# Kernel optimization log

Measured on AMD Instinct MI355X. Metric: run time of the kernel, lower is better.

## Reference

```python
import jax, jax.numpy as jnp
import numpy as np

DIM, NH = 256, 8
B, L_INNER, L_LEAF, L_ROOT = 16, 128, 64, 16


def mha(q, k, v, wi, bi, wo, bo, nh=NH):
    # Faithful torch.nn.MultiheadAttention (batch_first): packed in_proj, q scaled by head_dim**-0.5.
    E = q.shape[-1]
    hd = E // nh
    wq, wk, wv = wi[:E], wi[E:2 * E], wi[2 * E:]
    bq, bk, bv = bi[:E], bi[E:2 * E], bi[2 * E:]

    def proj(x, w, b):
        Bx, Lx, _ = x.shape
        return (x @ w.T + b).reshape(Bx, Lx, nh, hd).transpose(0, 2, 1, 3)  # [B,H,L,hd]

    qh = proj(q, wq, bq) * (float(hd) ** -0.5)
    kh = proj(k, wk, bk)
    vh = proj(v, wv, bv)
    attn = jax.nn.softmax(jnp.einsum('bhqd,bhkd->bhqk', qh, kh), axis=-1)
    o = jnp.einsum('bhqk,bhkd->bhqd', attn, vh).transpose(0, 2, 1, 3).reshape(q.shape)
    return o @ wo.T + bo


def setup_inputs() -> dict:
    key = jax.random.key(0)
    ks = jax.random.split(key, 10)
    return {
        'leaf': jax.random.normal(ks[0], (B * L_INNER, L_LEAF, DIM), jnp.float32),
        'inner': jax.random.normal(ks[1], (B, L_INNER, DIM), jnp.float32),
        'root': jax.random.normal(ks[2], (B, L_ROOT, DIM), jnp.float32),
        'w_in': jax.random.normal(ks[3], (7, 3 * DIM, DIM), jnp.float32) * 0.02,
        'b_in': jax.random.normal(ks[4], (7, 3 * DIM), jnp.float32) * 0.02,
        'w_out': jax.random.normal(ks[5], (7, DIM, DIM), jnp.float32) * 0.02,
        'b_out': jax.random.normal(ks[6], (7, DIM), jnp.float32) * 0.02,
        'weight_leaf': jax.random.normal(ks[7], (2,), jnp.float32),
        'weight_inner': jax.random.normal(ks[8], (3,), jnp.float32),
        'weight_root': jax.random.normal(ks[9], (2,), jnp.float32),
    }


def reference(leaf, inner, root, w_in, b_in, w_out, b_out, weight_leaf, weight_inner, weight_root):
    # param slots: 0 leaf_parents, 1 leaf_siblings, 2 inner_parents, 3 inner_siblings,
    #              4 inner_children, 5 root_siblings, 6 root_children (constructed but UNUSED, as in source)
    inner_flat = inner.reshape(-1, 1, DIM)  # [B*L_inner, 1, dim]

    leaf_p = mha(leaf, inner_flat, inner_flat, w_in[0], b_in[0], w_out[0], b_out[0])
    leaf_s = mha(leaf, leaf, leaf, w_in[1], b_in[1], w_out[1], b_out[1])
    wl = jax.nn.softmax(weight_leaf)
    leaf_out = wl[0] * leaf_p + wl[1] * leaf_s

    inner_p = mha(inner, root, root, w_in[2], b_in[2], w_out[2], b_out[2])
    inner_s = mha(inner, inner, inner, w_in[3], b_in[3], w_out[3], b_out[3])
    inner_c = mha(inner_flat, leaf, leaf, w_in[4], b_in[4], w_out[4], b_out[4]).reshape(inner.shape)
    wi_ = jax.nn.softmax(weight_inner)
    inner_out = wi_[0] * inner_p + wi_[1] * inner_s + wi_[2] * inner_c

    root_s = mha(root, root, root, w_in[5], b_in[5], w_out[5], b_out[5])
    # source bug reproduced: root_c also uses attn_root_siblings (slot 5)
    root_c = mha(root, inner, inner, w_in[5], b_in[5], w_out[5], b_out[5])
    wr = jax.nn.softmax(weight_root)
    root_out = wr[0] * root_s + wr[1] * root_c

    return (leaf_out, inner_out, root_out)
```

## Files before the change

kernel.cpp:

```cpp
#include <hip/hip_runtime.h>
#include <hip/hip_bf16.h>
#include <cstdint>


#define DIM 256
#define NH 8
#define HD 32

static constexpr float SCALE = 0.17677669529663687f;

typedef __bf16 bf16x8 __attribute__((ext_vector_type(8)));
typedef __bf16 bf16x4 __attribute__((ext_vector_type(4)));
typedef float  f32x4  __attribute__((ext_vector_type(4)));

__device__ __forceinline__ float dot4(const float4 a, const float4 b) {
    return a.x * b.x + a.y * b.y + a.z * b.z + a.w * b.w;
}

__global__ __launch_bounds__(256) void cvt_f2b(const float* __restrict__ s,
                                               __bf16* __restrict__ d, int n) {
    int i = (blockIdx.x * 256 + threadIdx.x) * 4;
    if (i < n) {
        float4 v = *(const float4*)(s + i);
        d[i + 0] = (__bf16)v.x; d[i + 1] = (__bf16)v.y;
        d[i + 2] = (__bf16)v.z; d[i + 3] = (__bf16)v.w;
    }
}

__device__ void mega2_body(int g,
    const float* __restrict__ X, const float* __restrict__ inner,
    const __bf16* __restrict__ W1b, const float* __restrict__ Bi1,
    const __bf16* __restrict__ W4kvb, const float* __restrict__ W4q,
    const float* __restrict__ Bi4, __bf16* __restrict__ O1,
    float* __restrict__ Oc, char* __restrict__ smem)
{
    const int xcd  = g & 7;
    const int idx  = g >> 3;
    const int b    = xcd * 256 + (idx >> 2);
    const int hg   = idx & 3;
    const int tid  = threadIdx.x;
    const int wid  = tid >> 6;
    const int lane = tid & 63;
    const int lr   = lane & 15;
    const int lk   = (lane >> 4) * 8;
    const int prow = (lane >> 4) * 4;

    __bf16* Xs  = (__bf16*)smem;
    __bf16* Pw  = (__bf16*)(smem + wid * 2304);
    float* qpart = (float*)(smem + 9216);
    float* qv    = qpart + 256;
    float* psm   = qv + 64;
    float* opart = psm + 128;
    __bf16* Qs  = (__bf16*)(smem + 33792);
    __bf16* Ks  = (__bf16*)(smem + 43008);
    __bf16* Vt  = (__bf16*)(smem + 52224);
    __bf16* K4t = (__bf16*)(smem + 61440);
    __bf16* V4t = (__bf16*)(smem + 70656);

    {
        const float* xb = X + (size_t)b * 64 * DIM;
#pragma unroll
        for (int it = 0; it < 16; ++it) {
            const int e4 = it * 1024 + tid * 4;
            const f32x4 v = __builtin_nontemporal_load((const f32x4*)(xb + e4));
            bf16x4 t4;
            t4[0] = (__bf16)v[0]; t4[1] = (__bf16)v[1];
            t4[2] = (__bf16)v[2]; t4[3] = (__bf16)v[3];
            const int row = e4 >> 8, col = e4 & 255;
            *(bf16x4*)(Xs + row * 264 + col) = t4;
        }
    }
    __syncthreads();

    bf16x8 af[4][8];
#pragma unroll
    for (int tg = 0; tg < 4; ++tg)
#pragma unroll
        for (int kk = 0; kk < 8; ++kk)
            af[tg][kk] = *(const bf16x8*)(Xs + (size_t)(tg * 16 + lr) * 264 + kk * 32 + lk);

    {
        auto wsrc = [&](int t) -> const __bf16* {
            if (t < 12) {
                const int sec = t >> 2, sub = t & 3;
                return W1b + (size_t)(sec * 256 + hg * 64 + sub * 16) * DIM;
            }
            const int u = t - 12, sec = u >> 2, sub = u & 3;
            return W4kvb + (size_t)(sec * 256 + hg * 64 + sub * 16) * DIM;
        };
        const size_t boff = (size_t)lr * DIM + lk;
        const int t0w = wid * 5;
        bf16x8 bw[8], bn[8];
        {
            const __bf16* p = wsrc(t0w) + boff;
#pragma unroll
            for (int kk = 0; kk < 8; ++kk) bw[kk] = *(const bf16x8*)(p + kk * 32);
        }
        for (int i = 0; i < 5; ++i) {
            const int t = t0w + i;
            if (i + 1 < 5) {
                const __bf16* p = wsrc(t + 1) + boff;
#pragma unroll
                for (int kk = 0; kk < 8; ++kk) bn[kk] = *(const bf16x8*)(p + kk * 32);
            }
            f32x4 acc0 = {0.f,0.f,0.f,0.f}, acc1 = {0.f,0.f,0.f,0.f};
            f32x4 acc2 = {0.f,0.f,0.f,0.f}, acc3 = {0.f,0.f,0.f,0.f};
#pragma unroll
            for (int kk = 0; kk < 8; ++kk) {
                acc0 = __builtin_amdgcn_mfma_f32_16x16x32_bf16(af[0][kk], bw[kk], acc0, 0, 0, 0);
                acc1 = __builtin_amdgcn_mfma_f32_16x16x32_bf16(af[1][kk], bw[kk], acc1, 0, 0, 0);
                acc2 = __builtin_amdgcn_mfma_f32_16x16x32_bf16(af[2][kk], bw[kk], acc2, 0, 0, 0);
                acc3 = __builtin_amdgcn_mfma_f32_16x16x32_bf16(af[3][kk], bw[kk], acc3, 0, 0, 0);
            }
            f32x4 accT[4] = { acc0, acc1, acc2, acc3 };
            const int sub = t & 3;
            const int col = sub * 16 + lr;
            if (t < 4) {
                const float bias = Bi1[hg * 64 + sub * 16 + lr];
#pragma unroll
                for (int tg = 0; tg < 4; ++tg)
#pragma unroll
                    for (int r = 0; r < 4; ++r)
                        Qs[(size_t)(tg * 16 + prow + r) * 72 + col] =
                            (__bf16)((accT[tg][r] + bias) * SCALE);
            } else if (t < 8) {
                const float bias = Bi1[256 + hg * 64 + sub * 16 + lr];
#pragma unroll
                for (int tg = 0; tg < 4; ++tg)
#pragma unroll
                    for (int r = 0; r < 4; ++r)
                        Ks[(size_t)(tg * 16 + prow + r) * 72 + col] =
                            (__bf16)(accT[tg][r] + bias);
            } else if (t < 12) {
                const float bias = Bi1[512 + hg * 64 + sub * 16 + lr];
#pragma unroll
                for (int tg = 0; tg < 4; ++tg) {
                    bf16x4 pv;
#pragma unroll
                    for (int r = 0; r < 4; ++r) pv[r] = (__bf16)(accT[tg][r] + bias);
                    *(bf16x4*)(Vt + (size_t)col * 72 + tg * 16 + prow) = pv;
                }
            } else if (t < 16) {
                const float bias = Bi4[256 + hg * 64 + sub * 16 + lr];
#pragma unroll
                for (int tg = 0; tg < 4; ++tg) {
                    bf16x4 pv;
#pragma unroll
                    for (int r = 0; r < 4; ++r) pv[r] = (__bf16)(accT[tg][r] + bias);
                    *(bf16x4*)(K4t + (size_t)col * 72 + tg * 16 + prow) = pv;
                }
            } else {
                const float bias = Bi4[512 + hg * 64 + sub * 16 + lr];
#pragma unroll
                for (int tg = 0; tg < 4; ++tg) {
                    bf16x4 pv;
#pragma unroll
                    for (int r = 0; r < 4; ++r) pv[r] = (__bf16)(accT[tg][r] + bias);
                    *(bf16x4*)(V4t + (size_t)col * 72 + tg * 16 + prow) = pv;
                }
            }
#pragma unroll
            for (int kk = 0; kk < 8; ++kk) bw[kk] = bn[kk];
        }
    }
    __syncthreads();

    {
        const int o = tid & 63, part = tid >> 6;
        const float4* wr = (const float4*)(W4q + (size_t)(hg * 64 + o) * DIM + part * 64);
        const float4* xr = (const float4*)(inner + (size_t)b * DIM + part * 64);
        float accq = 0.f;
#pragma unroll
        for (int k = 0; k < 16; ++k) accq += dot4(xr[k], wr[k]);
        qpart[part * 64 + o] = accq;
    }
    __syncthreads();

    if (tid < 64)
        qv[tid] = (qpart[tid] + qpart[64 + tid] + qpart[128 + tid] + qpart[192 + tid]
                   + Bi4[hg * 64 + tid]) * SCALE;

    const int hh = wid >> 1;
    const int qh = wid & 1;
    f32x4 s[2][4];
    {
        bf16x8 kb[4];
#pragma unroll
        for (int kt = 0; kt < 4; ++kt)
            kb[kt] = *(const bf16x8*)(Ks + (size_t)(kt * 16 + lr) * 72 + hh * 32 + lk);
#pragma unroll
        for (int q2 = 0; q2 < 2; ++q2) {
            const int qt = qh * 2 + q2;
            const bf16x8 qa = *(const bf16x8*)(Qs + (size_t)(qt * 16 + lr) * 72 + hh * 32 + lk);
#pragma unroll
            for (int kt = 0; kt < 4; ++kt) {
                f32x4 z = {0.f, 0.f, 0.f, 0.f};
                s[q2][kt] = __builtin_amdgcn_mfma_f32_16x16x32_bf16(qa, kb[kt], z, 0, 0, 0);
            }
        }
    }
#pragma unroll
    for (int q2 = 0; q2 < 2; ++q2) {
#pragma unroll
        for (int r = 0; r < 4; ++r) {
            float m = fmaxf(fmaxf(s[q2][0][r], s[q2][1][r]), fmaxf(s[q2][2][r], s[q2][3][r]));
#pragma unroll
            for (int off = 1; off < 16; off <<= 1) m = fmaxf(m, __shfl_xor(m, off));
            const float p0 = __expf(s[q2][0][r] - m), p1 = __expf(s[q2][1][r] - m);
            const float p2 = __expf(s[q2][2][r] - m), p3 = __expf(s[q2][3][r] - m);
            float t = p0 + p1 + p2 + p3;
#pragma unroll
            for (int off = 1; off < 16; off <<= 1) t += __shfl_xor(t, off);
            const float inv = 1.0f / t;
            s[q2][0][r] = p0 * inv; s[q2][1][r] = p1 * inv;
            s[q2][2][r] = p2 * inv; s[q2][3][r] = p3 * inv;
        }
    }
    {
        bf16x8 vb[2][2];
#pragma unroll
        for (int dt = 0; dt < 2; ++dt)
#pragma unroll
            for (int ks = 0; ks < 2; ++ks)
                vb[dt][ks] = *(const bf16x8*)(Vt + (size_t)(hh * 32 + dt * 16 + lr) * 72 + ks * 32 + lk);
#pragma unroll
        for (int q2 = 0; q2 < 2; ++q2) {
            const int qt = qh * 2 + q2;
#pragma unroll
            for (int kt = 0; kt < 4; ++kt)
#pragma unroll
                for (int r = 0; r < 4; ++r)
                    Pw[(size_t)(prow + r) * 72 + kt * 16 + lr] = (__bf16)s[q2][kt][r];
            bf16x8 pa[2];
#pragma unroll
            for (int ks = 0; ks < 2; ++ks)
                pa[ks] = *(const bf16x8*)(Pw + (size_t)lr * 72 + ks * 32 + lk);
#pragma unroll
            for (int dt = 0; dt < 2; ++dt) {
                f32x4 o = {0.f, 0.f, 0.f, 0.f};
#pragma unroll
                for (int ks = 0; ks < 2; ++ks)
                    o = __builtin_amdgcn_mfma_f32_16x16x32_bf16(pa[ks], vb[dt][ks], o, 0, 0, 0);
                const int colO = (hg * 2 + hh) * 32 + dt * 16 + lr;
#pragma unroll
                for (int r = 0; r < 4; ++r)
                    __builtin_nontemporal_store((__bf16)o[r],
                        &O1[((size_t)b * 64 + qt * 16 + prow + r) * DIM + colO]);
            }
        }
    }
    __syncthreads();

    if (wid < 2) {
        const int j = lane;
        float sv = 0.f;
#pragma unroll
        for (int d = 0; d < 32; ++d)
            sv += qv[wid * 32 + d] * (float)K4t[(size_t)(wid * 32 + d) * 72 + j];
        float m = sv;
#pragma unroll
        for (int off = 1; off < 64; off <<= 1) m = fmaxf(m, __shfl_xor(m, off));
        const float p = __expf(sv - m);
        float t = p;
#pragma unroll
        for (int off = 1; off < 64; off <<= 1) t += __shfl_xor(t, off);
        psm[wid * 64 + j] = p / t;
    }
    __syncthreads();

    if (tid < 128) {
        const int o = tid & 63, hf = tid >> 6;
        const int ho = o >> 5;
        float acc2 = 0.f;
#pragma unroll
        for (int j = 0; j < 32; ++j)
            acc2 += psm[ho * 64 + hf * 32 + j] * (float)V4t[(size_t)o * 72 + hf * 32 + j];
        opart[hf * 64 + o] = acc2;
    }
    __syncthreads();
    if (tid < 64)
        Oc[(size_t)b * DIM + hg * 64 + tid] = opart[tid] + opart[64 + tid];
}

__device__ void leafp_mfma_body(int bid, const float* __restrict__ inner,
    const __bf16* __restrict__ Wv0b, const __bf16* __restrict__ Wo0b,
    const float* __restrict__ b_in0, const float* __restrict__ b_out0,
    float* __restrict__ tP, char* __restrict__ smem)
{
    __bf16* tV = (__bf16*)smem;
    __bf16* Bs = (__bf16*)(smem + 33792);
    const int tid  = threadIdx.x;
    const int wid  = tid >> 6;
    const int lane = tid & 63;
    const int lr   = lane & 15;
    const int lk   = (lane >> 4) * 8;
    const int prow = (lane >> 4) * 4;
    const int tok0 = wid * 16 + prow;
    const int srow = tid >> 5;
    const int scol = (tid & 31) * 8;

    bf16x8 a[8];
    {
        const float* xrow = inner + ((size_t)bid * 64 + wid * 16 + lr) * DIM + lk;
#pragma unroll
        for (int k = 0; k < 8; ++k) {
            float4 v0 = *(const float4*)(xrow + k * 32);
            float4 v1 = *(const float4*)(xrow + k * 32 + 4);
            bf16x8 t;
            t[0] = (__bf16)v0.x; t[1] = (__bf16)v0.y; t[2] = (__bf16)v0.z; t[3] = (__bf16)v0.w;
            t[4] = (__bf16)v1.x; t[5] = (__bf16)v1.y; t[6] = (__bf16)v1.z; t[7] = (__bf16)v1.w;
            a[k] = t;
        }
    }

    {
        bf16x8 g0 = *(const bf16x8*)(Wv0b + (size_t)srow * DIM + scol);
        bf16x8 g1 = *(const bf16x8*)(Wv0b + (size_t)(8 + srow) * DIM + scol);
        *(bf16x8*)(Bs + srow * 264 + scol) = g0;
        *(bf16x8*)(Bs + (8 + srow) * 264 + scol) = g1;
    }
    __syncthreads();
    for (int t = 0; t < 16; ++t) {
        const int cur = t & 1;
        const __bf16* Bc = Bs + cur * 4224;
        bf16x8 g0, g1;
        if (t + 1 < 16) {
            const __bf16* p = Wv0b + (size_t)((t + 1) * 16) * DIM;
            g0 = *(const bf16x8*)(p + (size_t)srow * DIM + scol);
            g1 = *(const bf16x8*)(p + (size_t)(8 + srow) * DIM + scol);
        }
        f32x4 acc = {0.f, 0.f, 0.f, 0.f};
#pragma unroll
        for (int k = 0; k < 8; ++k)
            acc = __builtin_amdgcn_mfma_f32_16x16x32_bf16(
                a[k], *(const bf16x8*)(Bc + lr * 264 + k * 32 + lk), acc, 0, 0, 0);
        const float bias = b_in0[512 + t * 16 + lr];
#pragma unroll
        for (int r = 0; r < 4; ++r)
            tV[(size_t)(tok0 + r) * 264 + t * 16 + lr] = (__bf16)(acc[r] + bias);
        if (t + 1 < 16) {
            __bf16* Bn = Bs + (cur ^ 1) * 4224;
            *(bf16x8*)(Bn + srow * 264 + scol) = g0;
            *(bf16x8*)(Bn + (8 + srow) * 264 + scol) = g1;
        }
        __syncthreads();
    }

    bf16x8 a2[8];
#pragma unroll
    for (int k = 0; k < 8; ++k)
        a2[k] = *(const bf16x8*)(tV + (size_t)(wid * 16 + lr) * 264 + k * 32 + lk);
    {
        bf16x8 g0 = *(const bf16x8*)(Wo0b + (size_t)srow * DIM + scol);
        bf16x8 g1 = *(const bf16x8*)(Wo0b + (size_t)(8 + srow) * DIM + scol);
        *(bf16x8*)(Bs + srow * 264 + scol) = g0;
        *(bf16x8*)(Bs + (8 + srow) * 264 + scol) = g1;
    }
    __syncthreads();
    for (int t = 0; t < 16; ++t) {
        const int cur = t & 1;
        const __bf16* Bc = Bs + cur * 4224;
        bf16x8 g0, g1;
        if (t + 1 < 16) {
            const __bf16* p = Wo0b + (size_t)((t + 1) * 16) * DIM;
            g0 = *(const bf16x8*)(p + (size_t)srow * DIM + scol);
            g1 = *(const bf16x8*)(p + (size_t)(8 + srow) * DIM + scol);
        }
        f32x4 acc = {0.f, 0.f, 0.f, 0.f};
#pragma unroll
        for (int k = 0; k < 8; ++k)
            acc = __builtin_amdgcn_mfma_f32_16x16x32_bf16(
                a2[k], *(const bf16x8*)(Bc + lr * 264 + k * 32 + lk), acc, 0, 0, 0);
        const float bo = b_out0[t * 16 + lr];
#pragma unroll
        for (int r = 0; r < 4; ++r)
            tP[((size_t)bid * 64 + wid * 16 + prow + r) * DIM + t * 16 + lr] = acc[r] + bo;
        if (t + 1 < 16) {
            __bf16* Bn = Bs + (cur ^ 1) * 4224;
            *(bf16x8*)(Bn + srow * 264 + scol) = g0;
            *(bf16x8*)(Bn + (8 + srow) * 264 + scol) = g1;
        }
        __syncthreads();
    }
}

template <int LQ, int LK, int RQ>
__device__ void attn_body(int bx, const float* __restrict__ Xq,
                          const float* __restrict__ Xkv,
                          const float* __restrict__ Wi, const float* __restrict__ Bi,
                          float* __restrict__ O, float* __restrict__ sm)
{
    const int b   = bx >> 3;
    const int h   = bx & 7;
    const int tid = threadIdx.x;

    float* KsP = sm;
    float* VsP = KsP + LK * 33;
    float* QsP = VsP + LK * 33;
    float* SP  = QsP + LQ * 33;

    const float* xq  = Xq  + (size_t)b * LQ * DIM;
    const float* xkv = Xkv + (size_t)b * LK * DIM;

    {
        const int col   = tid & 63;
        const int which = col >> 5;
        const int d     = col & 31;
        const int row   = DIM + which * DIM + h * HD + d;
        const float4* wr = (const float4*)(Wi + (size_t)row * DIM);
        const float bias = Bi[row];
        constexpr int TT = LK / 4;
        float acc[TT];
#pragma unroll
        for (int i = 0; i < TT; ++i) acc[i] = 0.f;
        const int t0 = tid >> 6;
        for (int k4 = 0; k4 < DIM / 4; ++k4) {
            const float4 w = wr[k4];
#pragma unroll
            for (int i = 0; i < TT; ++i) {
                const int t = t0 + 4 * i;
                const float4 aa = ((const float4*)(xkv + (size_t)t * DIM))[k4];
                acc[i] += dot4(aa, w);
            }
        }
#pragma unroll
        for (int i = 0; i < TT; ++i) {
            const int t = t0 + 4 * i;
            if (which == 0) KsP[t * 33 + d] = acc[i] + bias;
            else            VsP[t * 33 + d] = acc[i] + bias;
        }
    }
    {
        constexpr int TGQ = (LQ >= 8) ? 8 : LQ;
        constexpr int TT  = LQ / TGQ;
        if (tid < 32 * TGQ) {
            const int d   = tid & 31;
            const int row = h * HD + d;
            const float4* wr = (const float4*)(Wi + (size_t)row * DIM);
            const float bias = Bi[row];
            float acc[TT];
#pragma unroll
            for (int i = 0; i < TT; ++i) acc[i] = 0.f;
            const int t0 = tid >> 5;
            for (int k4 = 0; k4 < DIM / 4; ++k4) {
                const float4 w = wr[k4];
#pragma unroll
                for (int i = 0; i < TT; ++i) {
                    const int t = t0 + TGQ * i;
                    const float4 aa = ((const float4*)(xq + (size_t)t * DIM))[k4];
                    acc[i] += dot4(aa, w);
                }
            }
#pragma unroll
            for (int i = 0; i < TT; ++i) {
                const int t = t0 + TGQ * i;
                QsP[t * 33 + d] = (acc[i] + bias) * SCALE;
            }
        }
    }
    __syncthreads();

    for (int q0 = 0; q0 < LQ; q0 += RQ) {
        for (int idx = tid; idx < RQ * LK; idx += 256) {
            const int r = idx / LK;
            const int j = idx - r * LK;
            float acc = 0.f;
#pragma unroll
            for (int d = 0; d < HD; ++d)
                acc += QsP[(q0 + r) * 33 + d] * KsP[j * 33 + d];
            SP[r * (LK + 1) + j] = acc;
        }
        __syncthreads();
        if (tid < RQ * 8) {
            const int r   = tid >> 3;
            const int sub = tid & 7;
            float m = -1e30f;
            for (int j = sub; j < LK; j += 8) m = fmaxf(m, SP[r * (LK + 1) + j]);
#pragma unroll
            for (int off = 4; off; off >>= 1) m = fmaxf(m, __shfl_xor(m, off, 8));
            float sum = 0.f;
            for (int j = sub; j < LK; j += 8) {
                const float p = __expf(SP[r * (LK + 1) + j] - m);
                SP[r * (LK + 1) + j] = p;
                sum += p;
            }
#pragma unroll
            for (int off = 4; off; off >>= 1) sum += __shfl_xor(sum, off, 8);
            const float inv = 1.0f / sum;
            for (int j = sub; j < LK; j += 8) SP[r * (LK + 1) + j] *= inv;
        }
        __syncthreads();
        for (int idx = tid; idx < RQ * HD; idx += 256) {
            const int r = idx >> 5;
            const int d = idx & 31;
            float acc = 0.f;
            for (int j = 0; j < LK; ++j)
                acc += SP[r * (LK + 1) + j] * VsP[j * 33 + d];
            O[((size_t)(b * LQ + q0 + r)) * DIM + h * HD + d] = acc;
        }
        __syncthreads();
    }
}

__global__ __launch_bounds__(256, 2) void fused_main(
    const float* __restrict__ leaf, const float* __restrict__ inner,
    const float* __restrict__ root,
    const float* __restrict__ w_in, const float* __restrict__ b_in,
    const float* __restrict__ b_out,
    const __bf16* __restrict__ W1b, const __bf16* __restrict__ W4kvb,
    const __bf16* __restrict__ Wv0b, const __bf16* __restrict__ Wo0b,
    __bf16* __restrict__ O1, float* __restrict__ Oc, float* __restrict__ tP,
    float* __restrict__ Op, float* __restrict__ Osf,
    float* __restrict__ Ors, float* __restrict__ Orc)
{
    extern __shared__ __align__(16) char smem[];
    const int bid = blockIdx.x;
    const size_t WI = 768 * 256, BI = 768;
    if (bid < 128)
        attn_body<128, 128, 16>(bid, inner, inner, w_in + 3 * WI, b_in + 3 * BI,
                                Osf, (float*)smem);
    else if (bid < 256)
        attn_body<128, 16, 32>(bid - 128, inner, root, w_in + 2 * WI, b_in + 2 * BI,
                               Op, (float*)smem);
    else if (bid < 384)
        attn_body<16, 128, 16>(bid - 256, root, inner, w_in + 5 * WI, b_in + 5 * BI,
                               Orc, (float*)smem);
    else if (bid < 512)
        attn_body<16, 16, 16>(bid - 384, root, root, w_in + 5 * WI, b_in + 5 * BI,
                              Ors, (float*)smem);
    else if (bid < 544)
        leafp_mfma_body(bid - 512, inner, Wv0b, Wo0b, b_in, b_out, tP, smem);
    else
        mega2_body(bid - 544, leaf, inner, W1b, b_in + 1 * BI, W4kvb,
                   w_in + 4 * WI, b_in + 4 * BI, O1, Oc, smem);
}

__global__ __launch_bounds__(512) void combleaf_kernel(
    const __bf16* __restrict__ O1, const __bf16* __restrict__ Wo1,
    const float* __restrict__ Bo1, const float* __restrict__ tP,
    const float* __restrict__ wleaf, float* __restrict__ out)
{
    extern __shared__ __align__(16) char smem[];
    __bf16* Ws = (__bf16*)smem;
    const int bid  = blockIdx.x;
    const int tid  = threadIdx.x;
    const int wid  = tid >> 6;
    const int lane = tid & 63;
    const int lr   = lane & 15;
    const int lk   = (lane >> 4) * 8;
    const int prow = (lane >> 4) * 4;

    bf16x8 a[4][8];
#pragma unroll
    for (int tg = 0; tg < 4; ++tg) {
        const __bf16* ar = O1 + ((size_t)bid * 512 + wid * 64 + tg * 16 + lr) * DIM + lk;
#pragma unroll
        for (int k = 0; k < 8; ++k) a[tg][k] = *(const bf16x8*)(ar + k * 32);
    }
    {
        const int row = tid >> 1, hf = tid & 1;
        const __bf16* p = Wo1 + (size_t)row * DIM + hf * 128;
        __bf16* dst = Ws + (size_t)row * 264 + hf * 128;
#pragma unroll
        for (int q = 0; q < 16; ++q)
            *(bf16x8*)(dst + q * 8) = *(const bf16x8*)(p + q * 8);
    }
    __syncthreads();

    const float e0 = __expf(wleaf[0]), e1 = __expf(wleaf[1]);
    const float wl0 = e0 / (e0 + e1), wl1 = e1 / (e0 + e1);
    const int   tile = bid * 8 + wid;
    const size_t rb  = (size_t)bid * 512 + wid * 64;

    for (int nt = 0; nt < 16; ++nt) {
        bf16x8 bw[8];
#pragma unroll
        for (int k = 0; k < 8; ++k)
            bw[k] = *(const bf16x8*)(Ws + (size_t)(nt * 16 + lr) * 264 + k * 32 + lk);
        f32x4 acc0 = {0.f,0.f,0.f,0.f}, acc1 = {0.f,0.f,0.f,0.f};
        f32x4 acc2 = {0.f,0.f,0.f,0.f}, acc3 = {0.f,0.f,0.f,0.f};
#pragma unroll
        for (int k = 0; k < 8; ++k) {
            acc0 = __builtin_amdgcn_mfma_f32_16x16x32_bf16(a[0][k], bw[k], acc0, 0, 0, 0);
            acc1 = __builtin_amdgcn_mfma_f32_16x16x32_bf16(a[1][k], bw[k], acc1, 0, 0, 0);
            acc2 = __builtin_amdgcn_mfma_f32_16x16x32_bf16(a[2][k], bw[k], acc2, 0, 0, 0);
            acc3 = __builtin_amdgcn_mfma_f32_16x16x32_bf16(a[3][k], bw[k], acc3, 0, 0, 0);
        }
        f32x4 accT[4] = { acc0, acc1, acc2, acc3 };
        const int   o  = nt * 16 + lr;
        const float bo = Bo1[o];
        const float tv = tP[(size_t)tile * DIM + o];
#pragma unroll
        for (int tg = 0; tg < 4; ++tg)
#pragma unroll
            for (int r = 0; r < 4; ++r)
                out[(rb + tg * 16 + prow + r) * DIM + o] =
                    wl0 * tv + wl1 * (accT[tg][r] + bo);
    }
}

__device__ void combine_inner_body(int vb, const float* __restrict__ Op,
    const float* __restrict__ Osf, const float* __restrict__ Oc,
    const float* __restrict__ W2, const float* __restrict__ B2,
    const float* __restrict__ W3, const float* __restrict__ B3,
    const float* __restrict__ W4, const float* __restrict__ B4,
    const float* __restrict__ winner, float* __restrict__ out, float* __restrict__ Ts)
{
    const int n0 = vb * 32;
    const int o  = threadIdx.x;
    const float e0 = __expf(winner[0]), e1 = __expf(winner[1]), e2 = __expf(winner[2]);
    const float inv = 1.f / (e0 + e1 + e2);
    const float wt0 = e0 * inv, wt1 = e1 * inv, wt2 = e2 * inv;

    float acc[32];
#pragma unroll
    for (int r = 0; r < 32; ++r) acc[r] = 0.f;
    const float biasacc = wt0 * B2[o] + wt1 * B3[o] + wt2 * B4[o];

#pragma unroll
    for (int term = 0; term < 3; ++term) {
        const float* Ob = (term == 0) ? Op : (term == 1) ? Osf : Oc;
        const float* Wb = (term == 0) ? W2 : (term == 1) ? W3 : W4;
        const float wt  = (term == 0) ? wt0 : (term == 1) ? wt1 : wt2;
        __syncthreads();
        for (int idx = threadIdx.x; idx < 32 * DIM; idx += 256)
            Ts[idx] = Ob[(size_t)n0 * DIM + idx];
        __syncthreads();
        const float4* wr = (const float4*)(Wb + (size_t)o * DIM);
        for (int k4 = 0; k4 < DIM / 4; ++k4) {
            float4 w = wr[k4];
            w.x *= wt; w.y *= wt; w.z *= wt; w.w *= wt;
#pragma unroll
            for (int r = 0; r < 32; ++r) {
                const float4 aa = *(const float4*)&Ts[r * DIM + k4 * 4];
                acc[r] += dot4(aa, w);
            }
        }
    }
#pragma unroll
    for (int r = 0; r < 32; ++r)
        out[(size_t)(n0 + r) * DIM + o] = acc[r] + biasacc;
}

__device__ void combine_root_body(int vb, const float* __restrict__ Ors,
    const float* __restrict__ Orc, const float* __restrict__ W5,
    const float* __restrict__ B5, const float* __restrict__ wroot,
    float* __restrict__ out, float* __restrict__ Ts)
{
    const int n0 = vb * 32;
    const int o  = threadIdx.x;
    const float e0 = __expf(wroot[0]), e1 = __expf(wroot[1]);
    const float w0 = e0 / (e0 + e1), w1 = e1 / (e0 + e1);
    for (int idx = threadIdx.x; idx < 32 * DIM; idx += 256)
        Ts[idx] = w0 * Ors[(size_t)n0 * DIM + idx] + w1 * Orc[(size_t)n0 * DIM + idx];
    __syncthreads();
    float acc[32];
#pragma unroll
    for (int r = 0; r < 32; ++r) acc[r] = 0.f;
    const float4* wr = (const float4*)(W5 + (size_t)o * DIM);
    for (int k4 = 0; k4 < DIM / 4; ++k4) {
        const float4 w = wr[k4];
#pragma unroll
        for (int r = 0; r < 32; ++r) {
            const float4 aa = *(const float4*)&Ts[r * DIM + k4 * 4];
            acc[r] += dot4(aa, w);
        }
    }
    const float bo = B5[o];
#pragma unroll
    for (int r = 0; r < 32; ++r)
        out[(size_t)(n0 + r) * DIM + o] = acc[r] + bo;
}

__global__ __launch_bounds__(256) void combine_kernel(
    const float* __restrict__ w_out, const float* __restrict__ b_out,
    const float* __restrict__ Op, const float* __restrict__ Osf,
    const float* __restrict__ Oc, const float* __restrict__ Ors,
    const float* __restrict__ Orc, const float* __restrict__ winner,
    const float* __restrict__ wroot, float* __restrict__ out)
{
    extern __shared__ float smf[];
    const int bid = blockIdx.x;
    const size_t WO = 256 * 256, BO = 256;
    if (bid < 64)
        combine_inner_body(bid, Op, Osf, Oc,
                           w_out + 2 * WO, b_out + 2 * BO,
                           w_out + 3 * WO, b_out + 3 * BO,
                           w_out + 4 * WO, b_out + 4 * BO,
                           winner, out + 33554432, smf);
    else
        combine_root_body(bid - 64, Ors, Orc, w_out + 5 * WO, b_out + 5 * BO,
                          wroot, out + 33554432 + 524288, smf);
}

extern "C" void kernel_launch(void* const* d_in, const int* in_sizes, int n_in,
                              void* d_out, int out_size, void* d_ws, size_t ws_size,
                              hipStream_t stream)
{
    const float* leaf   = (const float*)d_in[0];
    const float* inner  = (const float*)d_in[1];
    const float* root   = (const float*)d_in[2];
    const float* w_in   = (const float*)d_in[3];
    const float* b_in   = (const float*)d_in[4];
    const float* w_out  = (const float*)d_in[5];
    const float* b_out  = (const float*)d_in[6];
    const float* wleaf  = (const float*)d_in[7];
    const float* winner = (const float*)d_in[8];
    const float* wroot  = (const float*)d_in[9];
    float* out = (float*)d_out;

    const size_t WI = 768 * 256, WO = 256 * 256;

    char* ws = (char*)d_ws;
    __bf16* W1b   = (__bf16*)(ws);
    __bf16* W4kvb = (__bf16*)(ws + 393216);
    __bf16* Wo1b  = (__bf16*)(ws + 655360);
    __bf16* Wv0b  = (__bf16*)(ws + 786432);
    __bf16* Wo0b  = (__bf16*)(ws + 917504);
    __bf16* O1b   = (__bf16*)(ws + 1048576);
    float*  tP    = (float*)(ws + 68157440);
    float*  Oc    = (float*)(ws + 70254592);
    float*  Op    = (float*)(ws + 72351744);
    float*  Osf   = (float*)(ws + 74448896);
    float*  Ors   = (float*)(ws + 76546048);
    float*  Orc   = (float*)(ws + 76808192);

    cvt_f2b<<<192, 256, 0, stream>>>(w_in + 1 * WI, W1b, 768 * 256);
    cvt_f2b<<<128, 256, 0, stream>>>(w_in + 4 * WI + 256 * 256, W4kvb, 512 * 256);
    cvt_f2b<<<64, 256, 0, stream>>>(w_out + 1 * WO, Wo1b, 256 * 256);
    cvt_f2b<<<64, 256, 0, stream>>>(w_in + 512 * 256, Wv0b, 256 * 256);
    cvt_f2b<<<64, 256, 0, stream>>>(w_out, Wo0b, 256 * 256);

    fused_main<<<8736, 256, 79872, stream>>>(
        leaf, inner, root, w_in, b_in, b_out, W1b, W4kvb, Wv0b, Wo0b,
        O1b, Oc, tP, Op, Osf, Ors, Orc);

    combleaf_kernel<<<256, 512, 135168, stream>>>(O1b, Wo1b, b_out + 256, tP,
                                                  wleaf, out);
    combine_kernel<<<72, 256, 32768, stream>>>(w_out, b_out, Op, Osf, Oc,
                                               Ors, Orc, winner, wroot, out);
}
```

Baseline: 681.3 us.

## Alias shared-memory buffers to raise occupancy and merge small launches

Reuses the same shared-memory region for the X staging tile, Q, K and the K4 buffers in the main fused kernel, with extra barriers to keep reuse safe. This shrinks dynamic LDS so three blocks can be resident per CU (launch bounds raised to 3). The attention body now projects Q per row chunk instead of for all rows up front, cutting its scratch size. The five weight-conversion launches are merged into one, and the two epilogue kernels into one 512-thread launch, with idle threads matching the barrier counts of the 256-thread bodies. The cost is extra syncs in the main kernel and register pressure from the higher occupancy target.

Result: slower. 923.3 us (+35.5%).

```diff
diff --git a/kernel.cpp b/kernel.cpp
--- a/kernel.cpp
+++ b/kernel.cpp
@@ -17,14 +17,29 @@
     return a.x * b.x + a.y * b.y + a.z * b.z + a.w * b.w;
 }
 
-__global__ __launch_bounds__(256) void cvt_f2b(const float* __restrict__ s,
-                                               __bf16* __restrict__ d, int n) {
-    int i = (blockIdx.x * 256 + threadIdx.x) * 4;
+__device__ __forceinline__ void cvt_range(const float* __restrict__ s,
+                                          __bf16* __restrict__ d, int lb, int n) {
+    int i = (lb * 256 + (int)threadIdx.x) * 4;
     if (i < n) {
         float4 v = *(const float4*)(s + i);
         d[i + 0] = (__bf16)v.x; d[i + 1] = (__bf16)v.y;
         d[i + 2] = (__bf16)v.z; d[i + 3] = (__bf16)v.w;
     }
+}
+
+__global__ __launch_bounds__(256) void cvt_all(
+    const float* __restrict__ w_in, const float* __restrict__ w_out,
+    __bf16* __restrict__ W1b, __bf16* __restrict__ W4kvb,
+    __bf16* __restrict__ Wo1b, __bf16* __restrict__ Wv0b,
+    __bf16* __restrict__ Wo0b)
+{
+    const size_t WI = 768 * 256, WO = 256 * 256;
+    const int bid = blockIdx.x;
+    if (bid < 192)       cvt_range(w_in + 1 * WI, W1b, bid, 768 * 256);
+    else if (bid < 320)  cvt_range(w_in + 4 * WI + 256 * 256, W4kvb, bid - 192, 512 * 256);
+    else if (bid < 384)  cvt_range(w_out + 1 * WO, Wo1b, bid - 320, 256 * 256);
+    else if (bid < 448)  cvt_range(w_in + 512 * 256, Wv0b, bid - 384, 256 * 256);
+    else                 cvt_range(w_out, Wo0b, bid - 448, 256 * 256);
 }
 
 __device__ void mega2_body(int g,
@@ -46,16 +61,16 @@
     const int prow = (lane >> 4) * 4;
 
     __bf16* Xs  = (__bf16*)smem;
+    __bf16* Qs  = (__bf16*)smem;
     __bf16* Pw  = (__bf16*)(smem + wid * 2304);
-    float* qpart = (float*)(smem + 9216);
+    __bf16* Ks  = (__bf16*)(smem + 9216);
+    __bf16* K4t = (__bf16*)(smem + 18432);
+    float* qpart = (float*)(smem + 27648);
     float* qv    = qpart + 256;
     float* psm   = qv + 64;
     float* opart = psm + 128;
-    __bf16* Qs  = (__bf16*)(smem + 33792);
-    __bf16* Ks  = (__bf16*)(smem + 43008);
-    __bf16* Vt  = (__bf16*)(smem + 52224);
-    __bf16* K4t = (__bf16*)(smem + 61440);
-    __bf16* V4t = (__bf16*)(smem + 70656);
+    __bf16* Vt  = (__bf16*)(smem + 33792);
+    __bf16* V4t = (__bf16*)(smem + 43008);
 
     {
         const float* xb = X + (size_t)b * 64 * DIM;
@@ -78,6 +93,7 @@
 #pragma unroll
         for (int kk = 0; kk < 8; ++kk)
             af[tg][kk] = *(const bf16x8*)(Xs + (size_t)(tg * 16 + lr) * 264 + kk * 32 + lk);
+    __syncthreads();
 
     {
         auto wsrc = [&](int t) -> const __bf16* {
@@ -216,13 +232,15 @@
             s[q2][2][r] = p2 * inv; s[q2][3][r] = p3 * inv;
         }
     }
-    {
-        bf16x8 vb[2][2];
-#pragma unroll
-        for (int dt = 0; dt < 2; ++dt)
-#pragma unroll
-            for (int ks = 0; ks < 2; ++ks)
-                vb[dt][ks] = *(const bf16x8*)(Vt + (size_t)(hh * 32 + dt * 16 + lr) * 72 + ks * 32 + lk);
+    bf16x8 vb[2][2];
+#pragma unroll
+    for (int dt = 0; dt < 2; ++dt)
+#pragma unroll
+        for (int ks = 0; ks < 2; ++ks)
+            vb[dt][ks] = *(const bf16x8*)(Vt + (size_t)(hh * 32 + dt * 16 + lr) * 72 + ks * 32 + lk);
+    __syncthreads();
+
+    {
 #pragma unroll
         for (int q2 = 0; q2 < 2; ++q2) {
             const int qt = qh * 2 + q2;
@@ -397,7 +415,7 @@
     float* KsP = sm;
     float* VsP = KsP + LK * 33;
     float* QsP = VsP + LK * 33;
-    float* SP  = QsP + LQ * 33;
+    float* SP  = QsP + RQ * 33;
 
     const float* xq  = Xq  + (size_t)b * LQ * DIM;
     const float* xkv = Xkv + (size_t)b * LK * DIM;
@@ -430,44 +448,32 @@
             else            VsP[t * 33 + d] = acc[i] + bias;
         }
     }
-    {
-        constexpr int TGQ = (LQ >= 8) ? 8 : LQ;
-        constexpr int TT  = LQ / TGQ;
-        if (tid < 32 * TGQ) {
-            const int d   = tid & 31;
+    __syncthreads();
+
+    for (int q0 = 0; q0 < LQ; q0 += RQ) {
+        {
+            const int d  = tid & 31;
+            const int rg = tid >> 5;
             const int row = h * HD + d;
             const float4* wr = (const float4*)(Wi + (size_t)row * DIM);
             const float bias = Bi[row];
-            float acc[TT];
-#pragma unroll
-            for (int i = 0; i < TT; ++i) acc[i] = 0.f;
-            const int t0 = tid >> 5;
-            for (int k4 = 0; k4 < DIM / 4; ++k4) {
-                const float4 w = wr[k4];
-#pragma unroll
-                for (int i = 0; i < TT; ++i) {
-                    const int t = t0 + TGQ * i;
-                    const float4 aa = ((const float4*)(xq + (size_t)t * DIM))[k4];
-                    acc[i] += dot4(aa, w);
-                }
-            }
-#pragma unroll
-            for (int i = 0; i < TT; ++i) {
-                const int t = t0 + TGQ * i;
-                QsP[t * 33 + d] = (acc[i] + bias) * SCALE;
-            }
-        }
-    }
-    __syncthreads();
-
-    for (int q0 = 0; q0 < LQ; q0 += RQ) {
+#pragma unroll
+            for (int i = 0; i < RQ / 8; ++i) {
+                const int rloc = rg + 8 * i;
+                float acc = 0.f;
+                const float4* xr = (const float4*)(xq + (size_t)(q0 + rloc) * DIM);
+                for (int k4 = 0; k4 < DIM / 4; ++k4) acc += dot4(xr[k4], wr[k4]);
+                QsP[rloc * 33 + d] = (acc + bias) * SCALE;
+            }
+        }
+        __syncthreads();
         for (int idx = tid; idx < RQ * LK; idx += 256) {
             const int r = idx / LK;
             const int j = idx - r * LK;
             float acc = 0.f;
 #pragma unroll
             for (int d = 0; d < HD; ++d)
-                acc += QsP[(q0 + r) * 33 + d] * KsP[j * 33 + d];
+                acc += QsP[r * 33 + d] * KsP[j * 33 + d];
             SP[r * (LK + 1) + j] = acc;
         }
         __syncthreads();
@@ -502,7 +508,7 @@
     }
 }
 
-__global__ __launch_bounds__(256, 2) void fused_main(
+__global__ __launch_bounds__(256, 3) void fused_main(
     const float* __restrict__ leaf, const float* __restrict__ inner,
     const float* __restrict__ root,
     const float* __restrict__ w_in, const float* __restrict__ b_in,
@@ -535,14 +541,12 @@
                    w_in + 4 * WI, b_in + 4 * BI, O1, Oc, smem);
 }
 
-__global__ __launch_bounds__(512) void combleaf_kernel(
-    const __bf16* __restrict__ O1, const __bf16* __restrict__ Wo1,
-    const float* __restrict__ Bo1, const float* __restrict__ tP,
-    const float* __restrict__ wleaf, float* __restrict__ out)
-{
-    extern __shared__ __align__(16) char smem[];
+__device__ void combleaf_body(int bid, const __bf16* __restrict__ O1,
+    const __bf16* __restrict__ Wo1, const float* __restrict__ Bo1,
+    const float* __restrict__ tP, const float* __restrict__ wleaf,
+    float* __restrict__ out, char* __restrict__ smem)
+{
     __bf16* Ws = (__bf16*)smem;
-    const int bid  = blockIdx.x;
     const int tid  = threadIdx.x;
     const int wid  = tid >> 6;
     const int lane = tid & 63;
@@ -607,7 +611,7 @@
     const float* __restrict__ winner, float* __restrict__ out, float* __restrict__ Ts)
 {
     const int n0 = vb * 32;
-    const int o  = threadIdx.x;
+    const int o  = threadIdx.x & 255;
     const float e0 = __expf(winner[0]), e1 = __expf(winner[1]), e2 = __expf(winner[2]);
     const float inv = 1.f / (e0 + e1 + e2);
     const float wt0 = e0 * inv, wt1 = e1 * inv, wt2 = e2 * inv;
@@ -648,7 +652,7 @@
     float* __restrict__ out, float* __restrict__ Ts)
 {
     const int n0 = vb * 32;
-    const int o  = threadIdx.x;
+    const int o  = threadIdx.x & 255;
     const float e0 = __expf(wroot[0]), e1 = __expf(wroot[1]);
     const float w0 = e0 / (e0 + e1), w1 = e1 / (e0 + e1);
     for (int idx = threadIdx.x; idx < 32 * DIM; idx += 256)
@@ -672,25 +676,38 @@
         out[(size_t)(n0 + r) * DIM + o] = acc[r] + bo;
 }
 
-__global__ __launch_bounds__(256) void combine_kernel(
+__global__ __launch_bounds__(512) void epilogue_kernel(
+    const __bf16* __restrict__ O1, const __bf16* __restrict__ Wo1b,
     const float* __restrict__ w_out, const float* __restrict__ b_out,
-    const float* __restrict__ Op, const float* __restrict__ Osf,
-    const float* __restrict__ Oc, const float* __restrict__ Ors,
-    const float* __restrict__ Orc, const float* __restrict__ winner,
+    const float* __restrict__ tP, const float* __restrict__ Op,
+    const float* __restrict__ Osf, const float* __restrict__ Oc,
+    const float* __restrict__ Ors, const float* __restrict__ Orc,
+    const float* __restrict__ wleaf, const float* __restrict__ winner,
     const float* __restrict__ wroot, float* __restrict__ out)
 {
-    extern __shared__ float smf[];
+    extern __shared__ __align__(16) char smem[];
     const int bid = blockIdx.x;
     const size_t WO = 256 * 256, BO = 256;
-    if (bid < 64)
-        combine_inner_body(bid, Op, Osf, Oc,
-                           w_out + 2 * WO, b_out + 2 * BO,
-                           w_out + 3 * WO, b_out + 3 * BO,
-                           w_out + 4 * WO, b_out + 4 * BO,
-                           winner, out + 33554432, smf);
-    else
-        combine_root_body(bid - 64, Ors, Orc, w_out + 5 * WO, b_out + 5 * BO,
-                          wroot, out + 33554432 + 524288, smf);
+    if (bid < 256) {
+        combleaf_body(bid, O1, Wo1b, b_out + BO, tP, wleaf, out, smem);
+    } else if (bid < 320) {
+        if (threadIdx.x < 256)
+            combine_inner_body(bid - 256, Op, Osf, Oc,
+                               w_out + 2 * WO, b_out + 2 * BO,
+                               w_out + 3 * WO, b_out + 3 * BO,
+                               w_out + 4 * WO, b_out + 4 * BO,
+                               winner, out + 33554432, (float*)smem);
+        else {
+#pragma unroll
+            for (int i = 0; i < 6; ++i) __syncthreads();
+        }
+    } else {
+        if (threadIdx.x < 256)
+            combine_root_body(bid - 320, Ors, Orc, w_out + 5 * WO, b_out + 5 * BO,
+                              wroot, out + 33554432 + 524288, (float*)smem);
+        else
+            __syncthreads();
+    }
 }
 
 extern "C" void kernel_launch(void* const* d_in, const int* in_sizes, int n_in,
@@ -708,8 +725,6 @@
     const float* winner = (const float*)d_in[8];
     const float* wroot  = (const float*)d_in[9];
     float* out = (float*)d_out;
-
-    const size_t WI = 768 * 256, WO = 256 * 256;
 
     char* ws = (char*)d_ws;
     __bf16* W1b   = (__bf16*)(ws);
@@ -725,18 +740,13 @@
     float*  Ors   = (float*)(ws + 76546048);
     float*  Orc   = (float*)(ws + 76808192);
 
-    cvt_f2b<<<192, 256, 0, stream>>>(w_in + 1 * WI, W1b, 768 * 256);
-    cvt_f2b<<<128, 256, 0, stream>>>(w_in + 4 * WI + 256 * 256, W4kvb, 512 * 256);
-    cvt_f2b<<<64, 256, 0, stream>>>(w_out + 1 * WO, Wo1b, 256 * 256);
-    cvt_f2b<<<64, 256, 0, stream>>>(w_in + 512 * 256, Wv0b, 256 * 256);
-    cvt_f2b<<<64, 256, 0, stream>>>(w_out, Wo0b, 256 * 256);
-
-    fused_main<<<8736, 256, 79872, stream>>>(
+    cvt_all<<<512, 256, 0, stream>>>(w_in, w_out, W1b, W4kvb, Wo1b, Wv0b, Wo0b);
+
+    fused_main<<<8736, 256, 52224, stream>>>(
         leaf, inner, root, w_in, b_in, b_out, W1b, W4kvb, Wv0b, Wo0b,
         O1b, Oc, tP, Op, Osf, Ors, Orc);
 
-    combleaf_kernel<<<256, 512, 135168, stream>>>(O1b, Wo1b, b_out + 256, tP,
-                                                  wleaf, out);
-    combine_kernel<<<72, 256, 32768, stream>>>(w_out, b_out, Op, Osf, Oc,
-                                               Ors, Orc, winner, wroot, out);
-}
+    epilogue_kernel<<<328, 512, 135168, stream>>>(O1b, Wo1b, w_out, b_out, tP,
+                                                  Op, Osf, Oc, Ors, Orc,
+                                                  wleaf, winner, wroot, out);
+}
```
